# Kernel tuning notes

Hardware: AMD Instinct MI355X
Metric: run time of the kernel (lower is better)

Reference implementation:

```python
import jax, jax.numpy as jnp
import numpy as np

NUM_USER, BATCH, NUM_NT = 8, 16384, 128
T = 0.3  # SE threshold from the original module


def setup_inputs() -> dict:
    key = jax.random.key(0)
    k1, k2 = jax.random.split(key)
    h = jax.random.normal(k1, (NUM_USER, BATCH, NUM_NT), dtype=jnp.float32)
    v = jax.random.normal(k2, (NUM_USER, BATCH, NUM_NT), dtype=jnp.float32)
    N = jnp.ones((), dtype=jnp.float32)
    return {"h": h, "v": v, "N": N}


def reference(h, v, N):
    num_user, batch, num_nt = h.shape
    d = num_nt // 2
    # split real/imag halves into complex views
    h_c = jax.lax.complex(h[..., :d], h[..., d:])  # (user, batch, d)
    v_c = jax.lax.complex(v[..., :d], v[..., d:])  # (user, batch, d)
    # per-sample Frobenius norm over (user, d) and power scaling to sqrt(num_user)
    norms = jnp.sqrt(jnp.sum(jnp.real(v_c) ** 2 + jnp.imag(v_c) ** 2, axis=(0, 2)))  # (batch,)
    scale = jnp.sqrt(jnp.float32(num_user)) / norms
    v_scaled = v_c * scale[None, :, None]
    # signal: diag(h_user @ v_user^H) per sample == row-wise complex dot, with SCALED v
    S = jnp.abs(jnp.sum(h_c * jnp.conj(v_scaled), axis=-1)) ** 2  # (user, batch)
    # interference: original uses UNSCALED v[j] (faithful to source)
    A = jnp.einsum('ibt,jbt->ijb', h_c, jnp.conj(v_c))  # (user_i, user_j, batch)
    Iall = jnp.abs(A) ** 2
    Ip = jnp.sum(Iall, axis=1) - jnp.einsum('iib->ib', Iall)  # exclude j == i
    SINR = S / (Ip + N)
    R_user = jnp.log2(1.0 + SINR)  # (user, batch)
    R_per_user_p = jnp.mean(R_user, axis=1)  # (user,)
    # Rp = sum_i ( -R_user_i + 10^(T - R_user_i) ) per sample
    Rp = jnp.sum(10.0 ** (T - R_user) - R_user, axis=0)  # (batch,)
    return jnp.mean(Rp), R_per_user_p, jnp.sum(R_per_user_p)
```

## Files before the change

### kernel.cpp

```cpp
#include <hip/hip_runtime.h>
#include <hip/hip_bf16.h>


constexpr int U_    = 8;
constexpr int B_    = 16384;
constexpr int NT_   = 128;
constexpr int D_    = 64;
constexpr int ROWP_ = 132;
constexpr int NBLK_ = 1024;
constexpr int WPB_  = 4;
constexpr int TW_   = NBLK_ * WPB_;
constexpr int IT_   = B_ / TW_;
constexpr float T_THRESH = 0.3f;
constexpr float LOG2_10  = 3.3219280948873623f;

__device__ __forceinline__ float waveReduceSum(float v) {
    #pragma unroll
    for (int m = 1; m < 64; m <<= 1) v += __shfl_xor(v, m, 64);
    return v;
}

__global__ __launch_bounds__(256) void se_main(const float* __restrict__ h,
                                               const float* __restrict__ vv,
                                               const float* __restrict__ Np,
                                               float* __restrict__ partial) {
    __shared__ float lds[WPB_][2][U_ * ROWP_];
    __shared__ float red_f[WPB_];
    __shared__ float red_R[WPB_][U_];

    const int tid  = threadIdx.x;
    const int wave = tid >> 6;
    const int lane = tid & 63;
    const int ui   = lane >> 3;
    const int uj   = lane & 7;
    const float Nval = Np[0];

    float* hb = lds[wave][0];
    float* vb = lds[wave][1];

    float lane_sumR = 0.0f;
    float lane_sumf = 0.0f;

    const int gwave = blockIdx.x * WPB_ + wave;

    for (int it = 0; it < IT_; ++it) {
        const int b = gwave + it * TW_;

        float nsq = 0.0f;
        #pragma unroll
        for (int t = 0; t < 4; ++t) {
            const int idx = t * 64 + lane;
            const int row = idx >> 5;
            const int c4  = idx & 31;
            const size_t goff = (size_t)row * ((size_t)B_ * NT_) + (size_t)b * NT_ + (size_t)c4 * 4;
            const float4 h4 = *reinterpret_cast<const float4*>(h  + goff);
            const float4 v4 = *reinterpret_cast<const float4*>(vv + goff);
            *reinterpret_cast<float4*>(&hb[row * ROWP_ + c4 * 4]) = h4;
            *reinterpret_cast<float4*>(&vb[row * ROWP_ + c4 * 4]) = v4;
            nsq += v4.x * v4.x + v4.y * v4.y + v4.z * v4.z + v4.w * v4.w;
        }
        const float normsq = waveReduceSum(nsq);
        __syncthreads();

        float are = 0.0f, aim = 0.0f;
        const float* hrow = &hb[ui * ROWP_];
        const float* vrow = &vb[uj * ROWP_];
        #pragma unroll
        for (int k = 0; k < D_; k += 4) {
            const float4 hr = *reinterpret_cast<const float4*>(hrow + k);
            const float4 hi = *reinterpret_cast<const float4*>(hrow + D_ + k);
            const float4 vr = *reinterpret_cast<const float4*>(vrow + k);
            const float4 vi = *reinterpret_cast<const float4*>(vrow + D_ + k);
            are += hr.x * vr.x + hi.x * vi.x;
            aim += hi.x * vr.x - hr.x * vi.x;
            are += hr.y * vr.y + hi.y * vi.y;
            aim += hi.y * vr.y - hr.y * vi.y;
            are += hr.z * vr.z + hi.z * vi.z;
            aim += hi.z * vr.z - hr.z * vi.z;
            are += hr.w * vr.w + hi.w * vi.w;
            aim += hi.w * vr.w - hr.w * vi.w;
        }
        const float Iall = are * are + aim * aim;

        const float diag = __shfl(Iall, ui * 9, 64);
        float rowsum = Iall;
        rowsum += __shfl_xor(rowsum, 1, 64);
        rowsum += __shfl_xor(rowsum, 2, 64);
        rowsum += __shfl_xor(rowsum, 4, 64);

        const float Ip   = rowsum - diag;
        const float S    = (8.0f / normsq) * diag;
        const float SINR = S / (Ip + Nval);
        const float R    = log2f(1.0f + SINR);

        lane_sumR += R;
        lane_sumf += exp2f((T_THRESH - R) * LOG2_10) - R;
        __syncthreads();
    }

    const float wf = waveReduceSum(lane_sumf) * 0.125f;
    if (lane == 0) red_f[wave] = wf;
    if (uj == 0)   red_R[wave][ui] = lane_sumR;
    __syncthreads();

    if (tid < U_) {
        float s = 0.0f;
        #pragma unroll
        for (int w = 0; w < WPB_; ++w) s += red_R[w][tid];
        partial[blockIdx.x * 9 + 1 + tid] = s;
    } else if (tid == U_) {
        float s = 0.0f;
        #pragma unroll
        for (int w = 0; w < WPB_; ++w) s += red_f[w];
        partial[blockIdx.x * 9] = s;
    }
}

__global__ __launch_bounds__(256) void se_final(const float* __restrict__ partial,
                                                float* __restrict__ out) {
    __shared__ float sums[9];
    if (threadIdx.x < 9) sums[threadIdx.x] = 0.0f;
    __syncthreads();

    float local[9];
    #pragma unroll
    for (int s = 0; s < 9; ++s) local[s] = 0.0f;
    for (int b = threadIdx.x; b < NBLK_; b += 256) {
        #pragma unroll
        for (int s = 0; s < 9; ++s) local[s] += partial[b * 9 + s];
    }
    #pragma unroll
    for (int s = 0; s < 9; ++s) atomicAdd(&sums[s], local[s]);
    __syncthreads();

    if (threadIdx.x == 0) {
        const float inv = 1.0f / (float)B_;
        out[0] = sums[0] * inv;
        float tot = 0.0f;
        #pragma unroll
        for (int i = 0; i < U_; ++i) {
            const float r = sums[1 + i] * inv;
            out[1 + i] = r;
            tot += r;
        }
        out[9] = tot;
    }
}

extern "C" void kernel_launch(void* const* d_in, const int* in_sizes, int n_in,
                              void* d_out, int out_size, void* d_ws, size_t ws_size,
                              hipStream_t stream) {
    const float* h  = (const float*)d_in[0];
    const float* v  = (const float*)d_in[1];
    const float* Np = (const float*)d_in[2];
    float* out      = (float*)d_out;
    float* partial  = (float*)d_ws;

    se_main<<<NBLK_, 256, 0, stream>>>(h, v, Np, partial);
    se_final<<<1, 256, 0, stream>>>(partial, out);
}
```

Baseline: 172.0 us.

## Prefetch next sample into registers, drop barriers, use hardware log2/exp2

Global loads for the next batch sample are issued into registers while the current sample's complex dot products run out of LDS, so memory latency overlaps with compute. Both block-wide __syncthreads are removed, since each wave only touches its own LDS region. log2f/exp2f are replaced with the raw AMDGCN hardware intrinsics, and launch bounds now ask for four blocks per CU. The cost is higher register pressure, slightly less precise transcendental results, and relying on wave lockstep to order the LDS writes and reads.

```diff
diff --git a/kernel.cpp b/kernel.cpp
--- a/kernel.cpp
+++ b/kernel.cpp
@@ -20,10 +20,13 @@
     return v;
 }
 
-__global__ __launch_bounds__(256) void se_main(const float* __restrict__ h,
-                                               const float* __restrict__ vv,
-                                               const float* __restrict__ Np,
-                                               float* __restrict__ partial) {
+__device__ __forceinline__ float hw_log2(float x) { return __builtin_amdgcn_logf(x); }
+__device__ __forceinline__ float hw_exp2(float x) { return __builtin_amdgcn_exp2f(x); }
+
+__global__ __launch_bounds__(256, 4) void se_main(const float* __restrict__ h,
+                                                  const float* __restrict__ vv,
+                                                  const float* __restrict__ Np,
+                                                  float* __restrict__ partial) {
     __shared__ float lds[WPB_][2][U_ * ROWP_];
     __shared__ float red_f[WPB_];
     __shared__ float red_R[WPB_][U_];
@@ -38,29 +41,51 @@
     float* hb = lds[wave][0];
     float* vb = lds[wave][1];
 
+    int srow[4], sc4[4];
+    #pragma unroll
+    for (int t = 0; t < 4; ++t) {
+        const int idx = t * 64 + lane;
+        srow[t] = idx >> 5;
+        sc4[t]  = idx & 31;
+    }
+
     float lane_sumR = 0.0f;
     float lane_sumf = 0.0f;
 
     const int gwave = blockIdx.x * WPB_ + wave;
 
+    float4 hreg[4], vreg[4];
+    {
+        const int b = gwave;
+        #pragma unroll
+        for (int t = 0; t < 4; ++t) {
+            const size_t goff = (size_t)srow[t] * ((size_t)B_ * NT_) + (size_t)b * NT_ + (size_t)sc4[t] * 4;
+            hreg[t] = *reinterpret_cast<const float4*>(h  + goff);
+            vreg[t] = *reinterpret_cast<const float4*>(vv + goff);
+        }
+    }
+
     for (int it = 0; it < IT_; ++it) {
-        const int b = gwave + it * TW_;
-
         float nsq = 0.0f;
         #pragma unroll
+        for (int t = 0; t < 4; ++t)
+            nsq += vreg[t].x * vreg[t].x + vreg[t].y * vreg[t].y +
+                   vreg[t].z * vreg[t].z + vreg[t].w * vreg[t].w;
+        const float normsq = waveReduceSum(nsq);
+
+        #pragma unroll
         for (int t = 0; t < 4; ++t) {
-            const int idx = t * 64 + lane;
-            const int row = idx >> 5;
-            const int c4  = idx & 31;
-            const size_t goff = (size_t)row * ((size_t)B_ * NT_) + (size_t)b * NT_ + (size_t)c4 * 4;
-            const float4 h4 = *reinterpret_cast<const float4*>(h  + goff);
-            const float4 v4 = *reinterpret_cast<const float4*>(vv + goff);
-            *reinterpret_cast<float4*>(&hb[row * ROWP_ + c4 * 4]) = h4;
-            *reinterpret_cast<float4*>(&vb[row * ROWP_ + c4 * 4]) = v4;
-            nsq += v4.x * v4.x + v4.y * v4.y + v4.z * v4.z + v4.w * v4.w;
+            *reinterpret_cast<float4*>(&hb[srow[t] * ROWP_ + sc4[t] * 4]) = hreg[t];
+            *reinterpret_cast<float4*>(&vb[srow[t] * ROWP_ + sc4[t] * 4]) = vreg[t];
         }
-        const float normsq = waveReduceSum(nsq);
-        __syncthreads();
+
+        const int bn = (it + 1 < IT_) ? (gwave + (it + 1) * TW_) : gwave;
+        #pragma unroll
+        for (int t = 0; t < 4; ++t) {
+            const size_t goff = (size_t)srow[t] * ((size_t)B_ * NT_) + (size_t)bn * NT_ + (size_t)sc4[t] * 4;
+            hreg[t] = *reinterpret_cast<const float4*>(h  + goff);
+            vreg[t] = *reinterpret_cast<const float4*>(vv + goff);
+        }
 
         float are = 0.0f, aim = 0.0f;
         const float* hrow = &hb[ui * ROWP_];
@@ -91,11 +116,10 @@
         const float Ip   = rowsum - diag;
         const float S    = (8.0f / normsq) * diag;
         const float SINR = S / (Ip + Nval);
-        const float R    = log2f(1.0f + SINR);
+        const float R    = hw_log2(1.0f + SINR);
 
         lane_sumR += R;
-        lane_sumf += exp2f((T_THRESH - R) * LOG2_10) - R;
-        __syncthreads();
+        lane_sumf += hw_exp2((T_THRESH - R) * LOG2_10) - R;
     }
 
     const float wf = waveReduceSum(lane_sumf) * 0.125f;
```

Measured after the change: 192.4 us. 1.12x slower.
